# Kernel optimization log

Hardware: AMD Instinct MI355X
Metric: run time of the kernel (lower is better)

The kernel has to match this reference:

```python
import jax, jax.numpy as jnp
import numpy as np

EPS = 1e-4


def setup_inputs() -> dict:
    key = jax.random.key(0)
    k1, k2, k3, k4, k5 = jax.random.split(key, 5)
    N, M, F = 2048, 2048, 128
    embeds = jax.random.uniform(k1, (N, F), dtype=jnp.float32)
    base_embeds = jax.random.normal(k2, (M, F), dtype=jnp.float32)
    base_rewards = jax.random.normal(k3, (M,), dtype=jnp.float32)
    # torch Linear(num_feat, num_feat, bias=False) / Linear(num_feat, 1, bias=False)
    # stored here as [in, out] for x @ W convention
    W1 = jax.random.normal(k4, (F, F), dtype=jnp.float32) / np.sqrt(F)
    w2 = jax.random.normal(k5, (F, 1), dtype=jnp.float32) / np.sqrt(F)
    return {"embeds": embeds, "base_embeds": base_embeds,
            "base_rewards": base_rewards, "W1": W1, "w2": w2}


def reference(embeds, base_embeds, base_rewards, W1, w2):
    # pairwise differences: [N, M, F]
    diff = embeds[:, None, :] - base_embeds[None, :, :]
    # tiny MLP distance kernel: Linear -> ELU -> Linear, abs
    h = jax.nn.elu(jnp.einsum('nmf,fg->nmg', diff, W1))
    dist = jnp.abs(jnp.einsum('nmg,go->nmo', h, w2)[:, :, 0])  # [N, M]
    # inverse-distance normalized weights
    dist_w = 1.0 / (dist + EPS)
    dist_w = dist_w / jnp.sum(dist_w, axis=1, keepdims=True)
    rewards = jnp.sum(dist_w * base_rewards[None, :], axis=1)  # [N]
    return rewards
```

## Files before the change

kernel.cpp:

```cpp
#include <hip/hip_runtime.h>
#include <hip/hip_bf16.h>

#define F      128
#define NROWS  2048
#define MROWS  2048
#define BN     128
#define BM     64
#define MT     (MROWS/BM)
#define NCH    16
#define LOG2E  1.44269504088896340736f

#define ROWF       20
#define AB_FLOATS  (BN * ROWF)
#define BB_FLOATS  (BM * ROWF)
#define BUF_FLOATS (AB_FLOATS + BB_FLOATS)

typedef float f32x2 __attribute__((ext_vector_type(2)));
typedef float f32x4 __attribute__((ext_vector_type(4)));

__device__ __forceinline__ f32x2 lo2(f32x4 v) { return __builtin_shufflevector(v, v, 0, 1); }
__device__ __forceinline__ f32x2 hi2(f32x4 v) { return __builtin_shufflevector(v, v, 2, 3); }
__device__ __forceinline__ void gload16(const float* g, float* l) {
    __builtin_amdgcn_global_load_lds(
        (const __attribute__((address_space(1))) void*)g,
        (__attribute__((address_space(3))) void*)l, 16, 0, 0);
}

__global__ __launch_bounds__(256) void proj_kernel(
    const float* __restrict__ embeds, const float* __restrict__ base,
    const float* __restrict__ W1, const float* __restrict__ w2,
    float* __restrict__ PA, float* __restrict__ PB,
    float* __restrict__ w2sum)
{
    const int tid = threadIdx.x;
    const int sub = tid >> 7;
    const int g   = tid & 127;
    const int row = blockIdx.x * 2 + sub;

    __shared__ float xs[2][F];
    {
        const float* src = (row < NROWS) ? &embeds[(size_t)row * F]
                                         : &base[(size_t)(row - NROWS) * F];
        xs[sub][g] = src[g];
    }
    __syncthreads();

    float acc = 0.0f;
#pragma unroll 8
    for (int f = 0; f < F; ++f)
        acc = fmaf(xs[sub][f], W1[f * F + g], acc);

    const float wv = w2[g];
    const int   ch = g >> 3, o = g & 7;
    if (row < NROWS) {
        float* dst = PA + (size_t)row * 256 + ch * 16 + o;
        dst[0] = (acc + 1.0f) * wv;
        dst[8] = __builtin_amdgcn_exp2f(acc * LOG2E) * wv;
    } else {
        float* dst = PB + (size_t)(row - NROWS) * 256 + ch * 16 + o;
        dst[0] = -acc * wv;
        dst[8] = __builtin_amdgcn_exp2f(-acc * LOG2E);
    }

    if (blockIdx.x == 0 && tid < 64) {
        float s = w2[tid] + w2[tid + 64];
#pragma unroll
        for (int k = 1; k < 64; k <<= 1) s += __shfl_xor(s, k);
        if (tid == 0) *w2sum = s;
    }
}

__global__ __launch_bounds__(256, 2) void pair_kernel(
    const float* __restrict__ PA, const float* __restrict__ PB,
    const float* __restrict__ w2, const float* __restrict__ w2sum_p,
    const float* __restrict__ brew, float* __restrict__ partials)
{
    __shared__ float sbuf[2 * BUF_FLOATS];
    __shared__ float w2l[F];

    const int tid = threadIdx.x;
    const int wvi = tid >> 6, l = tid & 63;
    const int nt  = blockIdx.x, mt = blockIdx.y;
    const int n0  = nt * BN,    m0 = mt * BM;
    const int tr  = tid >> 4,   tc = tid & 15;

    const float* ssrc[4];
    int sdst[4];
#pragma unroll
    for (int t = 0; t < 4; ++t) {
        const int k = wvi + 4 * t;
        int slot, dstf;
        const float* basep;
        if (k < 10) { slot = 64 * k + l;        dstf = k * 256;                    basep = PA + (size_t)n0 * 256; }
        else        { slot = 64 * (k - 10) + l; dstf = AB_FLOATS + (k - 10) * 256; basep = PB + (size_t)m0 * 256; }
        const int row = slot / 5;
        const int rs  = slot - row * 5;
        const int rsd = (rs == 4) ? 0 : rs;
        ssrc[t] = basep + row * 256 + rsd * 4;
        sdst[t] = dstf;
    }
    const bool has3 = (wvi < 3);

#define STAGE(CH, BUF) {                                                       \
    gload16(ssrc[0] + (CH) * 16, &sbuf[(BUF) * BUF_FLOATS + sdst[0]]);         \
    gload16(ssrc[1] + (CH) * 16, &sbuf[(BUF) * BUF_FLOATS + sdst[1]]);         \
    gload16(ssrc[2] + (CH) * 16, &sbuf[(BUF) * BUF_FLOATS + sdst[2]]);         \
    if (has3)                                                                   \
        gload16(ssrc[3] + (CH) * 16, &sbuf[(BUF) * BUF_FLOATS + sdst[3]]); }

    float acc[8][4];
#pragma unroll
    for (int i = 0; i < 8; ++i)
#pragma unroll
        for (int j = 0; j < 4; ++j) acc[i][j] = 0.0f;

    STAGE(0, 0)
    if (tid < F) w2l[tid] = w2[tid];
    __syncthreads();

#pragma unroll 1
    for (int ch = 0; ch < NCH; ++ch) {
        const int buf = ch & 1;
        if (ch + 1 < NCH) STAGE(ch + 1, buf ^ 1)

        const float* sa  = &sbuf[buf * BUF_FLOATS];
        const float* sbb = sa + AB_FLOATS;

#pragma unroll
        for (int h = 0; h < 2; ++h) {
            const float wq0 = w2l[ch * 8 + h * 4 + 0];
            const float wq1 = w2l[ch * 8 + h * 4 + 1];
            const float wq2 = w2l[ch * 8 + h * 4 + 2];
            const float wq3 = w2l[ch * 8 + h * 4 + 3];
            f32x4 b1v[4], bev[4];
#pragma unroll
            for (int j = 0; j < 4; ++j) {
                const float* bp = sbb + (tc + 16 * j) * ROWF + h * 4;
                b1v[j] = *(const f32x4*)bp;
                bev[j] = *(const f32x4*)(bp + 8);
            }
#pragma unroll
            for (int i = 0; i < 8; ++i) {
                const float* ap = sa + (tr + 16 * i) * ROWF + h * 4;
                const f32x4 a1 = *(const f32x4*)ap;
                const f32x4 ae = *(const f32x4*)(ap + 8);
                const f32x2 a1l = lo2(a1), a1h = hi2(a1);
                const f32x2 ael = lo2(ae), aeh = hi2(ae);
#pragma unroll
                for (int j = 0; j < 4; ++j) {
                    const f32x2 xl = a1l + lo2(b1v[j]);
                    const f32x2 xh = a1h + hi2(b1v[j]);
                    const f32x2 el = ael * lo2(bev[j]);
                    const f32x2 eh = aeh * hi2(bev[j]);
                    const float s0 = __builtin_amdgcn_fmed3f(xl.x, el.x, wq0);
                    const float s1 = __builtin_amdgcn_fmed3f(xl.y, el.y, wq1);
                    const float s2 = __builtin_amdgcn_fmed3f(xh.x, eh.x, wq2);
                    const float s3 = __builtin_amdgcn_fmed3f(xh.y, eh.y, wq3);
                    acc[i][j] += (s0 + s1) + (s2 + s3);
                }
            }
        }
        __syncthreads();
    }
#undef STAGE

    const float w2sum = *w2sum_p;
    float rsv[4];
#pragma unroll
    for (int j = 0; j < 4; ++j) rsv[j] = brew[m0 + tc + 16 * j];

#pragma unroll
    for (int i = 0; i < 8; ++i) {
        float sw = 0.0f, swr = 0.0f;
#pragma unroll
        for (int j = 0; j < 4; ++j) {
            const float dist = fabsf(acc[i][j] - w2sum);
            const float wgt  = 1.0f / (dist + 1e-4f);
            sw += wgt;
            swr = fmaf(wgt, rsv[j], swr);
        }
#pragma unroll
        for (int k = 1; k < 16; k <<= 1) {
            sw  += __shfl_xor(sw, k);
            swr += __shfl_xor(swr, k);
        }
        if (tc == 0) {
            const int n = n0 + tr + 16 * i;
            partials[((size_t)n * MT + mt) * 2 + 0] = sw;
            partials[((size_t)n * MT + mt) * 2 + 1] = swr;
        }
    }
}

__global__ __launch_bounds__(256) void finalize_kernel(
    const float* __restrict__ partials, float* __restrict__ out)
{
    const int n = blockIdx.x * 256 + threadIdx.x;
    if (n < NROWS) {
        float sw = 0.0f, swr = 0.0f;
#pragma unroll
        for (int t = 0; t < MT; ++t) {
            sw  += partials[((size_t)n * MT + t) * 2 + 0];
            swr += partials[((size_t)n * MT + t) * 2 + 1];
        }
        out[n] = swr / sw;
    }
}

extern "C" void kernel_launch(void* const* d_in, const int* in_sizes, int n_in,
                              void* d_out, int out_size, void* d_ws, size_t ws_size,
                              hipStream_t stream)
{
    const float* embeds       = (const float*)d_in[0];
    const float* base_embeds  = (const float*)d_in[1];
    const float* base_rewards = (const float*)d_in[2];
    const float* W1           = (const float*)d_in[3];
    const float* w2           = (const float*)d_in[4];
    float* out = (float*)d_out;

    float* partials = (float*)d_ws;
    float* PA  = partials + (size_t)NROWS * MT * 2;
    float* PB  = PA + (size_t)NROWS * 256;
    float* w2s = PB + (size_t)MROWS * 256;

    proj_kernel<<<(NROWS + MROWS) / 2, 256, 0, stream>>>(
        embeds, base_embeds, W1, w2, PA, PB, w2s);

    dim3 grid2(NROWS / BN, MROWS / BM);
    pair_kernel<<<grid2, 256, 0, stream>>>(PA, PB, w2, w2s, base_rewards, partials);

    finalize_kernel<<<(NROWS + 255) / 256, 256, 0, stream>>>(partials, out);
}
```

Baseline: 74.35 us.

## Give each wave private LDS staging to replace block barriers with waitcnt

Each wave now stages its own A rows (the 32 n-rows it computes) and a private copy of the full B tile into a per-wave double buffer. The per-chunk __syncthreads is replaced by a wave-local s_waitcnt vmcnt(0), which removes block-wide barrier stalls between waves. In exchange, every wave loads B redundantly, so LDS use grows to 64KB per block and global-to-LDS traffic rises. The packed f32x2 add/mul is also replaced by scalar expressions. Correctness depends on the hardware waitcnt covering LDS-DMA completion without a barrier.

After: 76.06 us. 2.3% more time.

```diff
diff --git a/kernel.cpp b/kernel.cpp
--- a/kernel.cpp
+++ b/kernel.cpp
@@ -10,16 +10,14 @@
 #define NCH    16
 #define LOG2E  1.44269504088896340736f
 
-#define ROWF       20
-#define AB_FLOATS  (BN * ROWF)
-#define BB_FLOATS  (BM * ROWF)
-#define BUF_FLOATS (AB_FLOATS + BB_FLOATS)
-
-typedef float f32x2 __attribute__((ext_vector_type(2)));
+#define ROWF   20
+#define ABASE  0
+#define BBASE  768
+#define BUF_F  2048
+#define WAVE_F (2 * BUF_F)
+
 typedef float f32x4 __attribute__((ext_vector_type(4)));
 
-__device__ __forceinline__ f32x2 lo2(f32x4 v) { return __builtin_shufflevector(v, v, 0, 1); }
-__device__ __forceinline__ f32x2 hi2(f32x4 v) { return __builtin_shufflevector(v, v, 2, 3); }
 __device__ __forceinline__ void gload16(const float* g, float* l) {
     __builtin_amdgcn_global_load_lds(
         (const __attribute__((address_space(1))) void*)g,
@@ -75,38 +73,47 @@
     const float* __restrict__ w2, const float* __restrict__ w2sum_p,
     const float* __restrict__ brew, float* __restrict__ partials)
 {
-    __shared__ float sbuf[2 * BUF_FLOATS];
+    __shared__ float sbuf[4 * WAVE_F];
     __shared__ float w2l[F];
 
     const int tid = threadIdx.x;
-    const int wvi = tid >> 6, l = tid & 63;
+    const int w   = tid >> 6, l = tid & 63;
     const int nt  = blockIdx.x, mt = blockIdx.y;
     const int n0  = nt * BN,    m0 = mt * BM;
-    const int tr  = tid >> 4,   tc = tid & 15;
-
-    const float* ssrc[4];
-    int sdst[4];
-#pragma unroll
-    for (int t = 0; t < 4; ++t) {
-        const int k = wvi + 4 * t;
-        int slot, dstf;
+    const int tc  = tid & 15;
+    const int trw = (tid >> 4) & 3;
+    const int wbase = w * WAVE_F;
+
+    const float* ssrc[8];
+#pragma unroll
+    for (int t = 0; t < 8; ++t) {
+        int slot, row;
         const float* basep;
-        if (k < 10) { slot = 64 * k + l;        dstf = k * 256;                    basep = PA + (size_t)n0 * 256; }
-        else        { slot = 64 * (k - 10) + l; dstf = AB_FLOATS + (k - 10) * 256; basep = PB + (size_t)m0 * 256; }
-        const int row = slot / 5;
-        const int rs  = slot - row * 5;
-        const int rsd = (rs == 4) ? 0 : rs;
-        ssrc[t] = basep + row * 256 + rsd * 4;
-        sdst[t] = dstf;
-    }
-    const bool has3 = (wvi < 3);
-
-#define STAGE(CH, BUF) {                                                       \
-    gload16(ssrc[0] + (CH) * 16, &sbuf[(BUF) * BUF_FLOATS + sdst[0]]);         \
-    gload16(ssrc[1] + (CH) * 16, &sbuf[(BUF) * BUF_FLOATS + sdst[1]]);         \
-    gload16(ssrc[2] + (CH) * 16, &sbuf[(BUF) * BUF_FLOATS + sdst[2]]);         \
-    if (has3)                                                                   \
-        gload16(ssrc[3] + (CH) * 16, &sbuf[(BUF) * BUF_FLOATS + sdst[3]]); }
+        if (t < 3) {
+            slot = t * 64 + l;
+            const int rl = slot / 5;
+            row = n0 + 4 * w + (rl & 3) + 16 * (rl >> 2);
+            basep = PA;
+        } else {
+            slot = (t - 3) * 64 + l;
+            row = m0 + slot / 5;
+            basep = PB;
+        }
+        int rs = slot - (slot / 5) * 5;
+        if (rs == 4) rs = 0;
+        ssrc[t] = basep + (size_t)row * 256 + rs * 4;
+    }
+
+#define STAGE(CH, BUF) {                                                   \
+    float* db = &sbuf[wbase + (BUF) * BUF_F];                              \
+    gload16(ssrc[0] + (CH) * 16, db +    0);                               \
+    gload16(ssrc[1] + (CH) * 16, db +  256);                               \
+    gload16(ssrc[2] + (CH) * 16, db +  512);                               \
+    gload16(ssrc[3] + (CH) * 16, db +  768);                               \
+    gload16(ssrc[4] + (CH) * 16, db + 1024);                               \
+    gload16(ssrc[5] + (CH) * 16, db + 1280);                               \
+    gload16(ssrc[6] + (CH) * 16, db + 1536);                               \
+    gload16(ssrc[7] + (CH) * 16, db + 1792); }
 
     float acc[8][4];
 #pragma unroll
@@ -123,8 +130,8 @@
         const int buf = ch & 1;
         if (ch + 1 < NCH) STAGE(ch + 1, buf ^ 1)
 
-        const float* sa  = &sbuf[buf * BUF_FLOATS];
-        const float* sbb = sa + AB_FLOATS;
+        const float* sa  = &sbuf[wbase + buf * BUF_F];
+        const float* sbb = sa + BBASE;
 
 #pragma unroll
         for (int h = 0; h < 2; ++h) {
@@ -141,26 +148,20 @@
             }
 #pragma unroll
             for (int i = 0; i < 8; ++i) {
-                const float* ap = sa + (tr + 16 * i) * ROWF + h * 4;
+                const float* ap = sa + (i * 4 + trw) * ROWF + h * 4;
                 const f32x4 a1 = *(const f32x4*)ap;
                 const f32x4 ae = *(const f32x4*)(ap + 8);
-                const f32x2 a1l = lo2(a1), a1h = hi2(a1);
-                const f32x2 ael = lo2(ae), aeh = hi2(ae);
 #pragma unroll
                 for (int j = 0; j < 4; ++j) {
-                    const f32x2 xl = a1l + lo2(b1v[j]);
-                    const f32x2 xh = a1h + hi2(b1v[j]);
-                    const f32x2 el = ael * lo2(bev[j]);
-                    const f32x2 eh = aeh * hi2(bev[j]);
-                    const float s0 = __builtin_amdgcn_fmed3f(xl.x, el.x, wq0);
-                    const float s1 = __builtin_amdgcn_fmed3f(xl.y, el.y, wq1);
-                    const float s2 = __builtin_amdgcn_fmed3f(xh.x, eh.x, wq2);
-                    const float s3 = __builtin_amdgcn_fmed3f(xh.y, eh.y, wq3);
+                    const float s0 = __builtin_amdgcn_fmed3f(a1.x + b1v[j].x, ae.x * bev[j].x, wq0);
+                    const float s1 = __builtin_amdgcn_fmed3f(a1.y + b1v[j].y, ae.y * bev[j].y, wq1);
+                    const float s2 = __builtin_amdgcn_fmed3f(a1.z + b1v[j].z, ae.z * bev[j].z, wq2);
+                    const float s3 = __builtin_amdgcn_fmed3f(a1.w + b1v[j].w, ae.w * bev[j].w, wq3);
                     acc[i][j] += (s0 + s1) + (s2 + s3);
                 }
             }
         }
-        __syncthreads();
+        asm volatile("s_waitcnt vmcnt(0)" ::: "memory");
     }
 #undef STAGE
 
@@ -185,7 +186,7 @@
             swr += __shfl_xor(swr, k);
         }
         if (tc == 0) {
-            const int n = n0 + tr + 16 * i;
+            const int n = n0 + (4 * w + trw) + 16 * i;
             partials[((size_t)n * MT + mt) * 2 + 0] = sw;
             partials[((size_t)n * MT + mt) * 2 + 1] = swr;
         }
```

## Split feature reduction across two thread groups per block with LDS combine

Applied to the files above, without the earlier changes.

Doubles the pair kernel block to 512 threads. Each 256-thread group handles half of the 16 feature chunks with its own double-buffered LDS region, and the two partial accumulators are merged through shared memory before the weighting epilogue. This shortens the serial chunk loop per thread and adds more waves for latency hiding. The cost is extra LDS use, an added barrier and combine step, and tighter register limits from launch_bounds(512,4). The inner loop also drops the packed f32x2 formulation in favour of scalar ops, which may change how the compiler emits packed math.

Result: slower. 291.6 us (+292.1%).

```diff
diff --git a/kernel.cpp b/kernel.cpp
--- a/kernel.cpp
+++ b/kernel.cpp
@@ -7,19 +7,16 @@
 #define BN     128
 #define BM     64
 #define MT     (MROWS/BM)
-#define NCH    16
 #define LOG2E  1.44269504088896340736f
 
-#define ROWF       20
-#define AB_FLOATS  (BN * ROWF)
-#define BB_FLOATS  (BM * ROWF)
-#define BUF_FLOATS (AB_FLOATS + BB_FLOATS)
-
-typedef float f32x2 __attribute__((ext_vector_type(2)));
+#define ROWF   20
+#define AB_F   (BN * ROWF)
+#define BB_F   (BM * ROWF)
+#define BUF_F  (AB_F + BB_F)
+#define GRP_F  (2 * BUF_F)
+
 typedef float f32x4 __attribute__((ext_vector_type(4)));
 
-__device__ __forceinline__ f32x2 lo2(f32x4 v) { return __builtin_shufflevector(v, v, 0, 1); }
-__device__ __forceinline__ f32x2 hi2(f32x4 v) { return __builtin_shufflevector(v, v, 2, 3); }
 __device__ __forceinline__ void gload16(const float* g, float* l) {
     __builtin_amdgcn_global_load_lds(
         (const __attribute__((address_space(1))) void*)g,
@@ -70,19 +67,22 @@
     }
 }
 
-__global__ __launch_bounds__(256, 2) void pair_kernel(
+__global__ __launch_bounds__(512, 4) void pair_kernel(
     const float* __restrict__ PA, const float* __restrict__ PB,
     const float* __restrict__ w2, const float* __restrict__ w2sum_p,
     const float* __restrict__ brew, float* __restrict__ partials)
 {
-    __shared__ float sbuf[2 * BUF_FLOATS];
+    __shared__ float sbuf[4 * BUF_F];
     __shared__ float w2l[F];
 
     const int tid = threadIdx.x;
-    const int wvi = tid >> 6, l = tid & 63;
+    const int G   = tid >> 8;
+    const int tl  = tid & 255;
+    const int wvi = tl >> 6, l = tid & 63;
     const int nt  = blockIdx.x, mt = blockIdx.y;
     const int n0  = nt * BN,    m0 = mt * BM;
-    const int tr  = tid >> 4,   tc = tid & 15;
+    const int tr  = tl >> 4,    tc = tl & 15;
+    const int gbase = G * GRP_F;
 
     const float* ssrc[4];
     int sdst[4];
@@ -91,22 +91,22 @@
         const int k = wvi + 4 * t;
         int slot, dstf;
         const float* basep;
-        if (k < 10) { slot = 64 * k + l;        dstf = k * 256;                    basep = PA + (size_t)n0 * 256; }
-        else        { slot = 64 * (k - 10) + l; dstf = AB_FLOATS + (k - 10) * 256; basep = PB + (size_t)m0 * 256; }
+        if (k < 10) { slot = 64 * k + l;        dstf = k * 256;               basep = PA + (size_t)n0 * 256; }
+        else        { slot = 64 * (k - 10) + l; dstf = AB_F + (k - 10) * 256; basep = PB + (size_t)m0 * 256; }
         const int row = slot / 5;
-        const int rs  = slot - row * 5;
-        const int rsd = (rs == 4) ? 0 : rs;
-        ssrc[t] = basep + row * 256 + rsd * 4;
+        int rs = slot - row * 5;
+        if (rs == 4) rs = 0;
+        ssrc[t] = basep + row * 256 + rs * 4;
         sdst[t] = dstf;
     }
     const bool has3 = (wvi < 3);
 
 #define STAGE(CH, BUF) {                                                       \
-    gload16(ssrc[0] + (CH) * 16, &sbuf[(BUF) * BUF_FLOATS + sdst[0]]);         \
-    gload16(ssrc[1] + (CH) * 16, &sbuf[(BUF) * BUF_FLOATS + sdst[1]]);         \
-    gload16(ssrc[2] + (CH) * 16, &sbuf[(BUF) * BUF_FLOATS + sdst[2]]);         \
-    if (has3)                                                                   \
-        gload16(ssrc[3] + (CH) * 16, &sbuf[(BUF) * BUF_FLOATS + sdst[3]]); }
+    float* db = &sbuf[gbase + (BUF) * BUF_F];                                  \
+    gload16(ssrc[0] + (CH) * 16, db + sdst[0]);                                \
+    gload16(ssrc[1] + (CH) * 16, db + sdst[1]);                                \
+    gload16(ssrc[2] + (CH) * 16, db + sdst[2]);                                \
+    if (has3) gload16(ssrc[3] + (CH) * 16, db + sdst[3]); }
 
     float acc[8][4];
 #pragma unroll
@@ -114,17 +114,18 @@
 #pragma unroll
         for (int j = 0; j < 4; ++j) acc[i][j] = 0.0f;
 
-    STAGE(0, 0)
+    STAGE(8 * G, 0)
     if (tid < F) w2l[tid] = w2[tid];
     __syncthreads();
 
 #pragma unroll 1
-    for (int ch = 0; ch < NCH; ++ch) {
-        const int buf = ch & 1;
-        if (ch + 1 < NCH) STAGE(ch + 1, buf ^ 1)
-
-        const float* sa  = &sbuf[buf * BUF_FLOATS];
-        const float* sbb = sa + AB_FLOATS;
+    for (int it = 0; it < 8; ++it) {
+        const int ch  = 8 * G + it;
+        const int buf = it & 1;
+        if (it + 1 < 8) STAGE(ch + 1, buf ^ 1)
+
+        const float* sa  = &sbuf[gbase + buf * BUF_F];
+        const float* sbb = sa + AB_F;
 
 #pragma unroll
         for (int h = 0; h < 2; ++h) {
@@ -144,18 +145,12 @@
                 const float* ap = sa + (tr + 16 * i) * ROWF + h * 4;
                 const f32x4 a1 = *(const f32x4*)ap;
                 const f32x4 ae = *(const f32x4*)(ap + 8);
-                const f32x2 a1l = lo2(a1), a1h = hi2(a1);
-                const f32x2 ael = lo2(ae), aeh = hi2(ae);
 #pragma unroll
                 for (int j = 0; j < 4; ++j) {
-                    const f32x2 xl = a1l + lo2(b1v[j]);
-                    const f32x2 xh = a1h + hi2(b1v[j]);
-                    const f32x2 el = ael * lo2(bev[j]);
-                    const f32x2 eh = aeh * hi2(bev[j]);
-                    const float s0 = __builtin_amdgcn_fmed3f(xl.x, el.x, wq0);
-                    const float s1 = __builtin_amdgcn_fmed3f(xl.y, el.y, wq1);
-                    const float s2 = __builtin_amdgcn_fmed3f(xh.x, eh.x, wq2);
-                    const float s3 = __builtin_amdgcn_fmed3f(xh.y, eh.y, wq3);
+                    const float s0 = __builtin_amdgcn_fmed3f(a1.x + b1v[j].x, ae.x * bev[j].x, wq0);
+                    const float s1 = __builtin_amdgcn_fmed3f(a1.y + b1v[j].y, ae.y * bev[j].y, wq1);
+                    const float s2 = __builtin_amdgcn_fmed3f(a1.z + b1v[j].z, ae.z * bev[j].z, wq2);
+                    const float s3 = __builtin_amdgcn_fmed3f(a1.w + b1v[j].w, ae.w * bev[j].w, wq3);
                     acc[i][j] += (s0 + s1) + (s2 + s3);
                 }
             }
@@ -164,30 +159,42 @@
     }
 #undef STAGE
 
-    const float w2sum = *w2sum_p;
-    float rsv[4];
-#pragma unroll
-    for (int j = 0; j < 4; ++j) rsv[j] = brew[m0 + tc + 16 * j];
-
-#pragma unroll
-    for (int i = 0; i < 8; ++i) {
-        float sw = 0.0f, swr = 0.0f;
-#pragma unroll
-        for (int j = 0; j < 4; ++j) {
-            const float dist = fabsf(acc[i][j] - w2sum);
-            const float wgt  = 1.0f / (dist + 1e-4f);
-            sw += wgt;
-            swr = fmaf(wgt, rsv[j], swr);
-        }
-#pragma unroll
-        for (int k = 1; k < 16; k <<= 1) {
-            sw  += __shfl_xor(sw, k);
-            swr += __shfl_xor(swr, k);
-        }
-        if (tc == 0) {
-            const int n = n0 + tr + 16 * i;
-            partials[((size_t)n * MT + mt) * 2 + 0] = sw;
-            partials[((size_t)n * MT + mt) * 2 + 1] = swr;
+    __syncthreads();
+    if (G == 1) {
+#pragma unroll
+        for (int i = 0; i < 8; ++i)
+            *(f32x4*)&sbuf[tl * 36 + i * 4] =
+                (f32x4){acc[i][0], acc[i][1], acc[i][2], acc[i][3]};
+    }
+    __syncthreads();
+    if (G == 0) {
+        const float w2sum = *w2sum_p;
+        float rsv[4];
+#pragma unroll
+        for (int j = 0; j < 4; ++j) rsv[j] = brew[m0 + tc + 16 * j];
+
+#pragma unroll
+        for (int i = 0; i < 8; ++i) {
+            const f32x4 o = *(const f32x4*)&sbuf[tl * 36 + i * 4];
+            float sw = 0.0f, swr = 0.0f;
+#pragma unroll
+            for (int j = 0; j < 4; ++j) {
+                const float tot  = acc[i][j] + o[j];
+                const float dist = fabsf(tot - w2sum);
+                const float wgt  = 1.0f / (dist + 1e-4f);
+                sw += wgt;
+                swr = fmaf(wgt, rsv[j], swr);
+            }
+#pragma unroll
+            for (int k = 1; k < 16; k <<= 1) {
+                sw  += __shfl_xor(sw, k);
+                swr += __shfl_xor(swr, k);
+            }
+            if (tc == 0) {
+                const int n = n0 + tr + 16 * i;
+                partials[((size_t)n * MT + mt) * 2 + 0] = sw;
+                partials[((size_t)n * MT + mt) * 2 + 1] = swr;
+            }
         }
     }
 }
@@ -227,7 +234,7 @@
         embeds, base_embeds, W1, w2, PA, PB, w2s);
 
     dim3 grid2(NROWS / BN, MROWS / BM);
-    pair_kernel<<<grid2, 256, 0, stream>>>(PA, PB, w2, w2s, base_rewards, partials);
+    pair_kernel<<<grid2, 512, 0, stream>>>(PA, PB, w2, w2s, base_rewards, partials);
 
     finalize_kernel<<<(NROWS + 255) / 256, 256, 0, stream>>>(partials, out);
 }
```
